# Kernel optimization log

Measured on AMD Instinct MI355X. Metric: run time of the kernel, lower is better.

Reference implementation:

```python
import jax, jax.numpy as jnp
import numpy as np

EPS = 1e-5

def conv3x3(x, w, b=None):
    # NCHW, OIHW, stride 1, padding 1
    y = jax.lax.conv_general_dilated(x, w, (1, 1), ((1, 1), (1, 1)),
                                     dimension_numbers=('NCHW', 'OIHW', 'NCHW'))
    if b is not None:
        y = y + b[None, :, None, None]
    return y

def batchnorm(x, g, b):
    # training-mode BN (PyTorch default): biased variance over (N,H,W)
    m = x.mean((0, 2, 3), keepdims=True)
    v = x.var((0, 2, 3), keepdims=True)
    return (x - m) * jax.lax.rsqrt(v + EPS) * g[None, :, None, None] + b[None, :, None, None]

def upsample2x_align_corners(x):
    # bilinear, align_corners=True, scale_factor=2
    def lerp_axis(a, Lin, axis):
        Lout = 2 * Lin
        c = jnp.arange(Lout, dtype=a.dtype) * (Lin - 1) / (Lout - 1)
        i0 = jnp.floor(c).astype(jnp.int32)
        i1 = jnp.minimum(i0 + 1, Lin - 1)
        w = c - i0.astype(a.dtype)
        shape = [1] * a.ndim
        shape[axis] = Lout
        w = w.reshape(shape)
        return jnp.take(a, i0, axis=axis) * (1 - w) + jnp.take(a, i1, axis=axis) * w
    x = lerp_axis(x, x.shape[2], 2)
    x = lerp_axis(x, x.shape[3], 3)
    return x

def deform_sample(x, offsets):
    # torchvision DeformConv2d v1 sampling: kernel 3x3, pad 1, offsets [B,18,H,W]
    # layout: per kernel point k (row-major), channels (2k, 2k+1) = (dy, dx)
    B, C, H, W = x.shape
    K = 9
    off = offsets.reshape(B, K, 2, H, W)
    ky, kx = jnp.meshgrid(jnp.arange(3) - 1, jnp.arange(3) - 1, indexing='ij')
    ky = ky.reshape(K).astype(x.dtype)
    kx = kx.reshape(K).astype(x.dtype)
    gy = jnp.arange(H, dtype=x.dtype)[None, None, :, None]
    gx = jnp.arange(W, dtype=x.dtype)[None, None, None, :]
    py = gy + ky[None, :, None, None] + off[:, :, 0]  # [B,K,H,W]
    px = gx + kx[None, :, None, None] + off[:, :, 1]
    y0 = jnp.floor(py)
    x0 = jnp.floor(px)
    wy = (py - y0)[:, None]  # [B,1,K,H,W]
    wx = (px - x0)[:, None]
    y0i = y0.astype(jnp.int32)
    x0i = x0.astype(jnp.int32)
    x_flat = x.reshape(B, C, H * W)
    def gather(yi, xi):
        valid = ((yi >= 0) & (yi < H) & (xi >= 0) & (xi < W))
        idx = jnp.clip(yi, 0, H - 1) * W + jnp.clip(xi, 0, W - 1)  # [B,K,H,W]
        g = jnp.take_along_axis(x_flat, idx.reshape(B, 1, K * H * W), axis=2)
        return g.reshape(B, C, K, H, W) * valid[:, None].astype(x.dtype)
    v00 = gather(y0i, x0i)
    v01 = gather(y0i, x0i + 1)
    v10 = gather(y0i + 1, x0i)
    v11 = gather(y0i + 1, x0i + 1)
    return (v00 * (1 - wy) * (1 - wx) + v01 * (1 - wy) * wx
            + v10 * wy * (1 - wx) + v11 * wy * wx)

def setup_inputs() -> dict:
    key = jax.random.key(0)
    ks = jax.random.split(key, 6)
    B, in_ch, skip_ch, out_ch = 4, 256, 128, 128
    Hs, Ws = 128, 128
    x = jax.random.normal(ks[0], (B, in_ch, Hs // 2, Ws // 2), jnp.float32)
    skip = jax.random.normal(ks[1], (B, skip_ch, Hs, Ws), jnp.float32)
    cat_ch = in_ch + skip_ch
    conv1_w = jax.random.normal(ks[2], (out_ch, cat_ch, 3, 3), jnp.float32) * (2.0 / (cat_ch * 9)) ** 0.5
    off_w = jax.random.normal(ks[3], (18, out_ch, 3, 3), jnp.float32) * 0.01
    off_b = jnp.zeros((18,), jnp.float32)
    def_w = jax.random.normal(ks[4], (out_ch, out_ch, 3, 3), jnp.float32) * (2.0 / (out_ch * 9)) ** 0.5
    def_b = jnp.zeros((out_ch,), jnp.float32)
    return {
        'x': x, 'skip': skip,
        'conv1_w': conv1_w,
        'bn1_g': jnp.ones((out_ch,), jnp.float32), 'bn1_b': jnp.zeros((out_ch,), jnp.float32),
        'off_w': off_w, 'off_b': off_b,
        'def_w': def_w, 'def_b': def_b,
        'bn2_g': jnp.ones((out_ch,), jnp.float32), 'bn2_b': jnp.zeros((out_ch,), jnp.float32),
    }

def reference(x, skip, conv1_w, bn1_g, bn1_b, off_w, off_b, def_w, def_b, bn2_g, bn2_b):
    xu = upsample2x_align_corners(x)
    dh = skip.shape[2] - xu.shape[2]
    dw = skip.shape[3] - xu.shape[3]
    if dh != 0 or dw != 0:
        xu = jnp.pad(xu, ((0, 0), (0, 0), (dh // 2, dh - dh // 2), (dw // 2, dw - dw // 2)))
    cat = jnp.concatenate([skip, xu], axis=1)
    h = jax.nn.relu(batchnorm(conv3x3(cat, conv1_w), bn1_g, bn1_b))
    offsets = conv3x3(h, off_w, off_b)  # [B,18,H,W]
    sampled = deform_sample(h, offsets)  # [B,C,9,H,W]
    O = def_w.shape[0]
    y = jnp.einsum('ock,bckhw->bohw', def_w.reshape(O, def_w.shape[1], 9), sampled)
    y = y + def_b[None, :, None, None]
    return jax.nn.relu(batchnorm(y, bn2_g, bn2_b))
```

## Files before the change

### kernel.cpp

```cpp
#include <hip/hip_runtime.h>
#include <hip/hip_bf16.h>

typedef __hip_bfloat16 bf16;
typedef __bf16 bf16x8 __attribute__((ext_vector_type(8)));
typedef __bf16 bf16x4 __attribute__((ext_vector_type(4)));
typedef float  f32x4  __attribute__((ext_vector_type(4)));

constexpr int NB   = 4;
constexpr int H    = 128;
constexpr int W    = 128;
constexpr int HW   = H * W;
constexpr int NPIX = NB * HW;
constexpr int CCAT = 384;
constexpr int CSKIP= 128;
constexpr int CIN  = 256;
constexpr int CO   = 128;
constexpr int HS   = 64;
constexpr int WP   = 130;
constexpr int K1   = 3456;
constexpr int KD   = 1152;
constexpr int NBORD= 2 * WP + 2 * (WP - 2);
constexpr float EPS = 1e-5f;

__device__ __forceinline__ float b2f(bf16 v){ return __bfloat162float(v); }
__device__ __forceinline__ bf16  f2b(float v){ return __float2bfloat16(v); }

__device__ __forceinline__ void async_copy16(const void* g, void* s){
    __builtin_amdgcn_global_load_lds((const __attribute__((address_space(1))) void*)g,
                                     (__attribute__((address_space(3))) void*)s, 16, 0, 0);
}

__device__ __forceinline__ void border_yx(int p, int& y, int& x){
    if (p < WP)             { y = 0;        x = p; }
    else if (p < 2 * WP)    { y = WP - 1;   x = p - WP; }
    else if (p < 2 * WP + (WP - 2)) { y = p - 2 * WP + 1;          x = 0; }
    else                    { y = p - (2 * WP + (WP - 2)) + 1;     x = WP - 1; }
}

__global__ void k_prep(float* __restrict__ sums, bf16* __restrict__ catp,
                       bf16* __restrict__ hp){
    int i = blockIdx.x * blockDim.x + threadIdx.x;
    int stride = gridDim.x * blockDim.x;
    for (int j = i; j < 512; j += stride) sums[j] = 0.f;
    const int nCat = NB * NBORD * CCAT;
    for (int j = i; j < nCat; j += stride){
        int c = j % CCAT, r = j / CCAT, p = r % NBORD, b = r / NBORD;
        int y, x; border_yx(p, y, x);
        catp[(((size_t)b * WP + y) * WP + x) * CCAT + c] = f2b(0.f);
    }
    const int nHp = NB * NBORD * CO;
    for (int j = i; j < nHp; j += stride){
        int c = j % CO, r = j / CO, p = r % NBORD, b = r / NBORD;
        int y, x; border_yx(p, y, x);
        hp[(((size_t)b * WP + y) * WP + x) * CO + c] = f2b(0.f);
    }
}

__global__ __launch_bounds__(256) void k_build_cat2(const float* __restrict__ x,
                                                    const float* __restrict__ skip,
                                                    bf16* __restrict__ catp){
    constexpr int TS = 66;
    __shared__ bf16 tile[128 * TS];
    int t  = threadIdx.x;
    int y  = blockIdx.x % H, b = blockIdx.x / H;
    int xx = t & 127, cp = t >> 7;

    float cy = (y * 63.0f) / 127.0f;
    int   y0 = (int)cy;
    int   y1 = min(y0 + 1, HS - 1);
    float wy = cy - y0;
    float cxf = (xx * 63.0f) / 127.0f;
    int   x0 = (int)cxf;
    int   x1 = min(x0 + 1, HS - 1);
    float wx = cxf - x0;

    bf16* orow = catp + (((size_t)b * WP + y + 1) * WP + 1) * CCAT;

    for (int chunk = 0; chunk < 6; chunk++){
        int cbase = chunk * 64;
        if (chunk >= 1) __syncthreads();
        if (chunk < 2){
            const float* sb = skip + ((size_t)(b * CSKIP + cbase + cp * 32) * H + y) * W;
#pragma unroll
            for (int i = 0; i < 32; i++)
                tile[xx * TS + cp * 32 + i] = f2b(sb[(size_t)i * HW + xx]);
        } else {
            int icb = (chunk - 2) * 64 + cp * 32;
            const float* xr0 = x + ((size_t)(b * CIN + icb) * HS + y0) * HS;
            const float* xr1 = x + ((size_t)(b * CIN + icb) * HS + y1) * HS;
#pragma unroll
            for (int i = 0; i < 32; i++){
                const float* r0 = xr0 + (size_t)i * HS * HS;
                const float* r1 = xr1 + (size_t)i * HS * HS;
                float v0 = r0[x0] * (1 - wx) + r0[x1] * wx;
                float v1 = r1[x0] * (1 - wx) + r1[x1] * wx;
                tile[xx * TS + cp * 32 + i] = f2b(v0 * (1 - wy) + v1 * wy);
            }
        }
        __syncthreads();
        int cc2 = (t & 31) * 2;
        int px0 = t >> 5;
#pragma unroll
        for (int pp = 0; pp < 16; pp++){
            int px = pp * 8 + px0;
            unsigned int v = *(const unsigned int*)&tile[px * TS + cc2];
            *(unsigned int*)&orow[(size_t)px * CCAT + cbase + cc2] = v;
        }
    }
}

__global__ void k_tr_all(const float* __restrict__ w1, const float* __restrict__ wo,
                         const float* __restrict__ wd,
                         bf16* __restrict__ wt1, bf16* __restrict__ wto,
                         bf16* __restrict__ wtd){
    int i = blockIdx.x * blockDim.x + threadIdx.x;
    if (i < CO * K1){
        int k = i % K1, oc = i / K1;
        int ky = k / 1152, r = k % 1152, kx = r / 384, ic = r % 384;
        wt1[i] = f2b(w1[((oc * CCAT + ic) * 3 + ky) * 3 + kx]);
        return;
    }
    i -= CO * K1;
    if (i < 32 * KD){
        int kk = i % KD, o = i / KD;
        int ky = kk / 384, r = kk % 384, kx = r >> 7, ic = r & 127;
        wto[i] = (o < 18) ? f2b(wo[((o * CO + ic) * 3 + ky) * 3 + kx]) : f2b(0.f);
        return;
    }
    i -= 32 * KD;
    if (i < CO * KD){
        int kk = i % KD, o = i / KD;
        int kp = kk >> 7, c = kk & 127;
        wtd[i] = f2b(wd[(o * CO + c) * 9 + kp]);
    }
}

__global__ __launch_bounds__(512) void k_conv1_mfma(const bf16* __restrict__ catp,
                                                    const bf16* __restrict__ wbt,
                                                    bf16* __restrict__ hp,
                                                    float* __restrict__ sums){
    __shared__ unsigned short Ab[256 * 64];
    __shared__ unsigned short Bb[128 * 64];
    __shared__ float ps[256];
    int t = threadIdx.x;
    int l = t & 63, w = t >> 6;
    int y0 = (blockIdx.x & 63) * 2, b = blockIdx.x >> 6;

    int pr   = l >> 3;
    int koct = (l & 7) ^ pr;
    int m    = l & 15, quad = l >> 4;
    int wm   = w & 3,  wn   = w >> 2;

    f32x4 acc[4][4];
#pragma unroll
    for (int i = 0; i < 4; i++)
#pragma unroll
        for (int j = 0; j < 4; j++) acc[i][j] = f32x4{0.f, 0.f, 0.f, 0.f};

    const size_t rowStride = (size_t)WP * CCAT;
    const bf16* Abase = catp + ((size_t)(b * WP) + y0) * rowStride;

    for (int ky = 0; ky < 3; ky++){
        for (int kc = 0; kc < 18; kc++){
            int c0 = kc / 6, r0 = (kc % 6) * 64;
            __syncthreads();
#pragma unroll
            for (int i = 0; i < 4; i++){
                int pxg = i * 64 + w * 8;
                int rr  = pxg >> 7;
                int xl  = (pxg & 127) + pr;
                const bf16* Arow = Abase + (size_t)(rr + ky) * rowStride;
                async_copy16(Arow + (size_t)(xl + c0) * CCAT + r0 + koct * 8,
                             &Ab[pxg * 64]);
            }
            int kg = ky * 1152 + kc * 64;
#pragma unroll
            for (int i = 0; i < 2; i++){
                int ocg = i * 64 + w * 8;
                async_copy16(wbt + (size_t)(ocg + pr) * K1 + kg + koct * 8,
                             &Bb[ocg * 64]);
            }
            __syncthreads();
            const bf16x8* ap = (const bf16x8*)Ab;
            const bf16x8* bp = (const bf16x8*)Bb;
#pragma unroll
            for (int ks = 0; ks < 2; ks++){
                bf16x8 af[4], bfr[4];
#pragma unroll
                for (int mi = 0; mi < 4; mi++){
                    int px = wm * 64 + mi * 16 + m;
                    af[mi] = ap[px * 8 + ((ks * 4 + quad) ^ (px & 7))];
                }
#pragma unroll
                for (int ni = 0; ni < 4; ni++){
                    int oc = wn * 64 + ni * 16 + m;
                    bfr[ni] = bp[oc * 8 + ((ks * 4 + quad) ^ (oc & 7))];
                }
#pragma unroll
                for (int mi = 0; mi < 4; mi++)
#pragma unroll
                    for (int ni = 0; ni < 4; ni++)
                        acc[mi][ni] = __builtin_amdgcn_mfma_f32_16x16x32_bf16(
                            af[mi], bfr[ni], acc[mi][ni], 0, 0, 0);
            }
        }
    }
#pragma unroll
    for (int mi = 0; mi < 4; mi++){
        int p0 = wm * 64 + mi * 16 + quad * 4;
        size_t obase = (((size_t)b * WP + y0 + (p0 >> 7) + 1) * WP + 1 + (p0 & 127)) * CO;
#pragma unroll
        for (int ni = 0; ni < 4; ni++){
            int oc = wn * 64 + ni * 16 + m;
#pragma unroll
            for (int r = 0; r < 4; r++)
                hp[obase + (size_t)r * CO + oc] = f2b(acc[mi][ni][r]);
        }
    }
    if (t < 256) ps[t] = 0.f;
    __syncthreads();
#pragma unroll
    for (int ni = 0; ni < 4; ni++){
        int ch = wn * 64 + ni * 16 + m;
        float s = 0.f, q = 0.f;
#pragma unroll
        for (int mi = 0; mi < 4; mi++)
#pragma unroll
            for (int r = 0; r < 4; r++){
                float v = acc[mi][ni][r];
                s += v; q += v * v;
            }
        s += __shfl_xor(s, 16); s += __shfl_xor(s, 32);
        q += __shfl_xor(q, 16); q += __shfl_xor(q, 32);
        if (quad == 0){
            atomicAdd(&ps[ch], s);
            atomicAdd(&ps[128 + ch], q);
        }
    }
    __syncthreads();
    if (t < 128){
        atomicAdd(&sums[t],       ps[t]);
        atomicAdd(&sums[128 + t], ps[128 + t]);
    }
}

__global__ __launch_bounds__(256) void k_bn_apply_pad(bf16* __restrict__ t,
                                                      const float* __restrict__ sums,
                                                      const float* __restrict__ g,
                                                      const float* __restrict__ bb){
    __shared__ float ssc[256];
    int tt = threadIdx.x;
    if (tt < 128){
        float mean = sums[tt] / (float)NPIX;
        float var  = sums[128 + tt] / (float)NPIX - mean * mean;
        float scale = g[tt] * rsqrtf(var + EPS);
        ssc[tt]       = scale;
        ssc[128 + tt] = bb[tt] - mean * scale;
    }
    __syncthreads();
    int i = blockIdx.x * 256 + tt;
    if (i >= NPIX * CO) return;
    int c = i & 127;
    int pix = i >> 7;
    int xw = pix & 127, yh = (pix >> 7) & 127, b = pix >> 14;
    size_t a = (((size_t)b * WP + yh + 1) * WP + xw + 1) * CO + c;
    float v = b2f(t[a]) * ssc[c] + ssc[128 + c];
    t[a] = f2b(v > 0.f ? v : 0.f);
}

__global__ __launch_bounds__(256) void k_conv_off_mfma(const bf16* __restrict__ hp,
                                                       const bf16* __restrict__ wob,
                                                       const float* __restrict__ off_b,
                                                       bf16* __restrict__ offs){
    __shared__ unsigned short Ab[128 * 64];
    __shared__ unsigned short Bb[32 * 64];
    int t = threadIdx.x, l = t & 63, w = t >> 6;
    int y = blockIdx.x % H, b = blockIdx.x / H;
    int pr = l >> 3, koct = (l & 7) ^ pr;
    int m = l & 15, quad = l >> 4;
    int wm = w & 1, wn = w >> 1;

    f32x4 acc[4];
#pragma unroll
    for (int i = 0; i < 4; i++) acc[i] = f32x4{0.f, 0.f, 0.f, 0.f};

    const size_t rowStride = (size_t)WP * CO;
    for (int ky = 0; ky < 3; ky++){
        const bf16* Arow = hp + ((size_t)(b * WP) + y + ky) * rowStride;
        for (int kc = 0; kc < 6; kc++){
            int kx = kc >> 1, r0 = (kc & 1) * 64;
            __syncthreads();
#pragma unroll
            for (int i = 0; i < 4; i++){
                int px = w * 32 + i * 8 + pr;
                async_copy16(Arow + (size_t)(px + kx) * CO + r0 + koct * 8,
                             &Ab[(w * 32 + i * 8) * 64]);
            }
            int kg = ky * 384 + kx * 128 + r0;
            async_copy16(wob + (size_t)(w * 8 + pr) * KD + kg + koct * 8,
                         &Bb[(w * 8) * 64]);
            __syncthreads();
            const bf16x8* ap = (const bf16x8*)Ab;
            const bf16x8* bp = (const bf16x8*)Bb;
#pragma unroll
            for (int ks = 0; ks < 2; ks++){
                int oc = wn * 16 + m;
                bf16x8 bfr = bp[oc * 8 + ((ks * 4 + quad) ^ (oc & 7))];
#pragma unroll
                for (int mi = 0; mi < 4; mi++){
                    int px = wm * 64 + mi * 16 + m;
                    bf16x8 af = ap[px * 8 + ((ks * 4 + quad) ^ (px & 7))];
                    acc[mi] = __builtin_amdgcn_mfma_f32_16x16x32_bf16(af, bfr, acc[mi], 0, 0, 0);
                }
            }
        }
    }
    int oc = wn * 16 + m;
    if (oc < 18){
        float bias = off_b[oc];
        int rowpix = b * HW + y * W;
#pragma unroll
        for (int mi = 0; mi < 4; mi++){
            int p0 = wm * 64 + mi * 16 + quad * 4;
#pragma unroll
            for (int r = 0; r < 4; r++)
                offs[(size_t)(rowpix + p0 + r) * 18 + oc] = f2b(acc[mi][r] + bias);
        }
    }
}

__global__ __launch_bounds__(256) void k_deform_mfma(const bf16* __restrict__ hp,
                                                     const bf16* __restrict__ offs,
                                                     const bf16* __restrict__ wdb,
                                                     const float* __restrict__ def_b,
                                                     bf16* __restrict__ y,
                                                     float* __restrict__ sums){
    __shared__ unsigned short Ab[128 * 64];
    __shared__ unsigned short Bb[128 * 64];
    __shared__ int2   sc_yx[9 * 128];
    __shared__ float4 sc_w[9 * 128];
    __shared__ float  ps[256];

    int t = threadIdx.x, l = t & 63, w = t >> 6;
    int yrow = blockIdx.x % H, b = blockIdx.x / H;
    int rowpix = b * HW + yrow * W;

    for (int idx = t; idx < 9 * 128; idx += 256){
        int kp = idx >> 7, px = idx & 127;
        float dy = b2f(offs[(size_t)(rowpix + px) * 18 + 2 * kp]);
        float dx = b2f(offs[(size_t)(rowpix + px) * 18 + 2 * kp + 1]);
        float py = yrow + (kp / 3 - 1) + dy;
        float pxx = px + (kp % 3 - 1) + dx;
        float fy = floorf(py), fx = floorf(pxx);
        float wy = py - fy, wx = pxx - fx;
        int y0 = (int)fy, x0 = (int)fx;
        bool vy0 = (y0 >= 0) && (y0 < H);
        bool vy1 = (y0 + 1 >= 0) && (y0 + 1 < H);
        bool vx0 = (x0 >= 0) && (x0 < W);
        bool vx1 = (x0 + 1 >= 0) && (x0 + 1 < W);
        int y0c = min(max(y0, 0), H - 1),     y1c = min(max(y0 + 1, 0), H - 1);
        int x0c = min(max(x0, 0), W - 1),     x1c = min(max(x0 + 1, 0), W - 1);
        sc_yx[idx] = make_int2(((y0c + 1) * WP) | (((y1c + 1) * WP) << 16),
                               (x0c + 1) | ((x1c + 1) << 16));
        sc_w[idx] = make_float4((1 - wy) * (1 - wx) * (float)(vy0 && vx0),
                                (1 - wy) * wx       * (float)(vy0 && vx1),
                                wy * (1 - wx)       * (float)(vy1 && vx0),
                                wy * wx             * (float)(vy1 && vx1));
    }
    __syncthreads();

    int pr = l >> 3, koct = (l & 7) ^ pr;
    int m = l & 15, quad = l >> 4;
    int wm = w & 1, wn = w >> 1;
    int g = l >> 4, j = l & 15;

    f32x4 acc[4][4];
#pragma unroll
    for (int i = 0; i < 4; i++)
#pragma unroll
        for (int jj = 0; jj < 4; jj++) acc[i][jj] = f32x4{0.f, 0.f, 0.f, 0.f};

    const bf16* hpb = hp + (size_t)b * WP * WP * CO;

    for (int kc = 0; kc < 18; kc++){
        int kp = kc >> 1, ch = (kc & 1) * 64;
        __syncthreads();
        int kg = kp * 128 + ch;
#pragma unroll
        for (int i = 0; i < 4; i++){
            int oc = w * 32 + i * 8 + pr;
            async_copy16(wdb + (size_t)oc * KD + kg + koct * 8,
                         &Bb[(w * 32 + i * 8) * 64]);
        }
        int cb = ch + j * 4;
#pragma unroll
        for (int p = 0; p < 8; p++){
            int px = w * 32 + g * 8 + p;
            int idx = kp * 128 + px;
            int2 yx = sc_yx[idx];
            float4 w4 = sc_w[idx];
            int r0 = yx.x & 0xffff, r1 = ((unsigned)yx.x) >> 16;
            int c0 = yx.y & 0xffff, c1 = ((unsigned)yx.y) >> 16;
            const bf16* base = hpb + cb;
            bf16x4 s00 = *(const bf16x4*)(base + (size_t)(r0 + c0) * CO);
            bf16x4 s01 = *(const bf16x4*)(base + (size_t)(r0 + c1) * CO);
            bf16x4 s10 = *(const bf16x4*)(base + (size_t)(r1 + c0) * CO);
            bf16x4 s11 = *(const bf16x4*)(base + (size_t)(r1 + c1) * CO);
            bf16x4 pv;
#pragma unroll
            for (int r = 0; r < 4; r++){
                float v = w4.x * (float)s00[r] + w4.y * (float)s01[r]
                        + w4.z * (float)s10[r] + w4.w * (float)s11[r];
                pv[r] = (__bf16)v;
            }
            int oct_sw = (j >> 1) ^ (px & 7);
            *(bf16x4*)&Ab[px * 64 + oct_sw * 8 + (j & 1) * 4] = pv;
        }
        __syncthreads();
        const bf16x8* ap = (const bf16x8*)Ab;
        const bf16x8* bp = (const bf16x8*)Bb;
#pragma unroll
        for (int ks = 0; ks < 2; ks++){
            bf16x8 af[4], bfr[4];
#pragma unroll
            for (int mi = 0; mi < 4; mi++){
                int px = wm * 64 + mi * 16 + m;
                af[mi] = ap[px * 8 + ((ks * 4 + quad) ^ (px & 7))];
            }
#pragma unroll
            for (int ni = 0; ni < 4; ni++){
                int oc = wn * 64 + ni * 16 + m;
                bfr[ni] = bp[oc * 8 + ((ks * 4 + quad) ^ (oc & 7))];
            }
#pragma unroll
            for (int mi = 0; mi < 4; mi++)
#pragma unroll
                for (int ni = 0; ni < 4; ni++)
                    acc[mi][ni] = __builtin_amdgcn_mfma_f32_16x16x32_bf16(
                        af[mi], bfr[ni], acc[mi][ni], 0, 0, 0);
        }
    }
#pragma unroll
    for (int mi = 0; mi < 4; mi++){
        int p0 = wm * 64 + mi * 16 + quad * 4;
#pragma unroll
        for (int ni = 0; ni < 4; ni++){
            int oc = wn * 64 + ni * 16 + m;
            float bias = def_b[oc];
#pragma unroll
            for (int r = 0; r < 4; r++)
                y[(size_t)(rowpix + p0 + r) * CO + oc] = f2b(acc[mi][ni][r] + bias);
        }
    }
    ps[t] = 0.f;
    __syncthreads();
#pragma unroll
    for (int ni = 0; ni < 4; ni++){
        int ch = wn * 64 + ni * 16 + m;
        float bias = def_b[ch];
        float s = 0.f, q = 0.f;
#pragma unroll
        for (int mi = 0; mi < 4; mi++)
#pragma unroll
            for (int r = 0; r < 4; r++){
                float v = acc[mi][ni][r] + bias;
                s += v; q += v * v;
            }
        s += __shfl_xor(s, 16); s += __shfl_xor(s, 32);
        q += __shfl_xor(q, 16); q += __shfl_xor(q, 32);
        if (quad == 0){
            atomicAdd(&ps[ch], s);
            atomicAdd(&ps[128 + ch], q);
        }
    }
    __syncthreads();
    if (t < 128){
        atomicAdd(&sums[t],       ps[t]);
        atomicAdd(&sums[128 + t], ps[128 + t]);
    }
}

__global__ __launch_bounds__(256) void k_final(const bf16* __restrict__ yb,
                                               const float* __restrict__ sums,
                                               const float* __restrict__ g,
                                               const float* __restrict__ bb,
                                               float* __restrict__ out){
    __shared__ unsigned short tile[128 * 129];
    __shared__ float ssc[256];
    int t = threadIdx.x;
    if (t < 128){
        float mean = sums[t] / (float)NPIX;
        float var  = sums[128 + t] / (float)NPIX - mean * mean;
        float scale = g[t] * rsqrtf(var + EPS);
        ssc[t]       = scale;
        ssc[128 + t] = bb[t] - mean * scale;
    }
    int yrow = blockIdx.x % H, b = blockIdx.x / H;
    int rowbase = b * HW + yrow * W;
    const unsigned short* src = (const unsigned short*)yb;
    for (int it = 0; it < 64; it++){
        int idx = it * 256 + t;
        int c = idx & 127, px = idx >> 7;
        tile[px * 129 + c] = src[(size_t)(rowbase + px) * CO + c];
    }
    __syncthreads();
    for (int it = 0; it < 64; it++){
        int idx = it * 256 + t;
        int xw = idx & 127, o = idx >> 7;
        unsigned short u = tile[xw * 129 + o];
        float v = (float)(*(const __bf16*)&u);
        v = v * ssc[o] + ssc[128 + o];
        out[(((size_t)b * CO + o) * H + yrow) * W + xw] = v > 0.f ? v : 0.f;
    }
}

extern "C" void kernel_launch(void* const* d_in, const int* in_sizes, int n_in,
                              void* d_out, int out_size, void* d_ws, size_t ws_size,
                              hipStream_t stream){
    const float* x      = (const float*)d_in[0];
    const float* skip   = (const float*)d_in[1];
    const float* conv1w = (const float*)d_in[2];
    const float* bn1g   = (const float*)d_in[3];
    const float* bn1b   = (const float*)d_in[4];
    const float* offw   = (const float*)d_in[5];
    const float* offb   = (const float*)d_in[6];
    const float* defw   = (const float*)d_in[7];
    const float* defb   = (const float*)d_in[8];
    const float* bn2g   = (const float*)d_in[9];
    const float* bn2b   = (const float*)d_in[10];
    float* out = (float*)d_out;

    char* ws = (char*)d_ws;
    size_t off_bytes = 0;
    auto alloc = [&](size_t bytes) -> void* {
        void* p = ws + off_bytes;
        off_bytes += (bytes + 255) & ~(size_t)255;
        return p;
    };
    const size_t catp_elems = (size_t)NB * WP * WP * CCAT;
    const size_t hp_elems   = (size_t)NB * WP * WP * CO;
    bf16*  catp  = (bf16*) alloc(catp_elems * 2);
    bf16*  hp    = (bf16*) alloc(hp_elems * 2);
    bf16*  offs  = (bf16*) alloc((size_t)NPIX * 18 * 2);
    bf16*  yb    = (bf16*) alloc((size_t)NPIX * CO * 2);
    bf16*  wbt   = (bf16*) alloc((size_t)CO * K1 * 2);
    bf16*  wob   = (bf16*) alloc((size_t)32 * KD * 2);
    bf16*  wdb   = (bf16*) alloc((size_t)CO * KD * 2);
    float* sums  = (float*)alloc(512 * 4);
    float* sums1 = sums;
    float* sums2 = sums + 256;

    k_prep<<<1024, 256, 0, stream>>>(sums, catp, hp);

    k_build_cat2<<<NB * H, 256, 0, stream>>>(x, skip, catp);

    const int ntr = CO * K1 + 32 * KD + CO * KD;
    k_tr_all<<<(ntr + 255) / 256, 256, 0, stream>>>(conv1w, offw, defw, wbt, wob, wdb);

    k_conv1_mfma<<<NB * H / 2, 512, 0, stream>>>(catp, wbt, hp, sums1);

    k_bn_apply_pad<<<(NPIX * CO + 255) / 256, 256, 0, stream>>>(hp, sums1, bn1g, bn1b);

    k_conv_off_mfma<<<NB * H, 256, 0, stream>>>(hp, wob, offb, offs);

    k_deform_mfma<<<NB * H, 256, 0, stream>>>(hp, offs, wdb, defb, yb, sums2);

    k_final<<<NB * H, 256, 0, stream>>>(yb, sums2, bn2g, bn2b, out);
}
```

Baseline: 359.3 us.

## Reuse haloed input row across kx taps in conv1 and offset conv

Both implicit-GEMM convolutions now load one padded input row (130 pixels plus a channel chunk) into shared memory once per ky/channel-chunk, then slide the pixel index by kx to cover all three horizontal taps. Previously each tap reloaded a separate A tile. This cuts global/LDS load traffic for activations about threefold. conv1 also changes from 512-thread blocks over two rows to 256-thread blocks over one row, and the offset conv loads all three kx weight slices at once. The cost is less parallelism per block, more barriers for the conv1 weight tiles, and larger LDS use.

```diff
diff --git a/kernel.cpp b/kernel.cpp
--- a/kernel.cpp
+++ b/kernel.cpp
@@ -135,21 +135,21 @@
     }
 }
 
-__global__ __launch_bounds__(512) void k_conv1_mfma(const bf16* __restrict__ catp,
+__global__ __launch_bounds__(256) void k_conv1_mfma(const bf16* __restrict__ catp,
                                                     const bf16* __restrict__ wbt,
                                                     bf16* __restrict__ hp,
                                                     float* __restrict__ sums){
-    __shared__ unsigned short Ab[256 * 64];
+    __shared__ unsigned short Ab[132 * 128];
     __shared__ unsigned short Bb[128 * 64];
     __shared__ float ps[256];
     int t = threadIdx.x;
     int l = t & 63, w = t >> 6;
-    int y0 = (blockIdx.x & 63) * 2, b = blockIdx.x >> 6;
+    int y = blockIdx.x % H, b = blockIdx.x / H;
 
     int pr   = l >> 3;
     int koct = (l & 7) ^ pr;
     int m    = l & 15, quad = l >> 4;
-    int wm   = w & 3,  wn   = w >> 2;
+    int wm   = w & 1,  wn   = w >> 1;
 
     f32x4 acc[4][4];
 #pragma unroll
@@ -158,66 +158,68 @@
         for (int j = 0; j < 4; j++) acc[i][j] = f32x4{0.f, 0.f, 0.f, 0.f};
 
     const size_t rowStride = (size_t)WP * CCAT;
-    const bf16* Abase = catp + ((size_t)(b * WP) + y0) * rowStride;
-
     for (int ky = 0; ky < 3; ky++){
-        for (int kc = 0; kc < 18; kc++){
-            int c0 = kc / 6, r0 = (kc % 6) * 64;
+        const bf16* Arow = catp + ((size_t)(b * WP) + y + ky) * rowStride;
+        for (int ci = 0; ci < 3; ci++){
             __syncthreads();
-#pragma unroll
-            for (int i = 0; i < 4; i++){
-                int pxg = i * 64 + w * 8;
-                int rr  = pxg >> 7;
-                int xl  = (pxg & 127) + pr;
-                const bf16* Arow = Abase + (size_t)(rr + ky) * rowStride;
-                async_copy16(Arow + (size_t)(xl + c0) * CCAT + r0 + koct * 8,
-                             &Ab[pxg * 64]);
-            }
-            int kg = ky * 1152 + kc * 64;
-#pragma unroll
-            for (int i = 0; i < 2; i++){
-                int ocg = i * 64 + w * 8;
-                async_copy16(wbt + (size_t)(ocg + pr) * K1 + kg + koct * 8,
-                             &Bb[ocg * 64]);
-            }
-            __syncthreads();
-            const bf16x8* ap = (const bf16x8*)Ab;
-            const bf16x8* bp = (const bf16x8*)Bb;
-#pragma unroll
-            for (int ks = 0; ks < 2; ks++){
-                bf16x8 af[4], bfr[4];
-#pragma unroll
-                for (int mi = 0; mi < 4; mi++){
-                    int px = wm * 64 + mi * 16 + m;
-                    af[mi] = ap[px * 8 + ((ks * 4 + quad) ^ (px & 7))];
+            for (int i = w; i < 33; i += 4){
+                int G  = i * 64 + l;
+                int px = G >> 4, ol = G & 15;
+                int osrc = ol ^ (px & 7);
+                async_copy16(Arow + (size_t)px * CCAT + ci * 128 + osrc * 8,
+                             &Ab[i * 512]);
+            }
+            for (int kx = 0; kx < 3; kx++){
+                for (int s64 = 0; s64 < 2; s64++){
+                    if (kx | s64) __syncthreads();
+                    int kg = ky * 1152 + kx * 384 + ci * 128 + s64 * 64;
+#pragma unroll
+                    for (int i = 0; i < 4; i++){
+                        int ocg = w * 32 + i * 8;
+                        async_copy16(wbt + (size_t)(ocg + pr) * K1 + kg + koct * 8,
+                                     &Bb[ocg * 64]);
+                    }
+                    __syncthreads();
+                    const bf16x8* ap = (const bf16x8*)Ab;
+                    const bf16x8* bp = (const bf16x8*)Bb;
+#pragma unroll
+                    for (int ks = 0; ks < 2; ks++){
+                        int s = s64 * 2 + ks;
+                        bf16x8 af[4], bfr[4];
+#pragma unroll
+                        for (int mi = 0; mi < 4; mi++){
+                            int pxk = wm * 64 + mi * 16 + m + kx;
+                            af[mi] = ap[pxk * 16 + ((s * 4 + quad) ^ (pxk & 7))];
+                        }
+#pragma unroll
+                        for (int ni = 0; ni < 4; ni++){
+                            int oc = wn * 64 + ni * 16 + m;
+                            bfr[ni] = bp[oc * 8 + ((ks * 4 + quad) ^ (oc & 7))];
+                        }
+#pragma unroll
+                        for (int mi = 0; mi < 4; mi++)
+#pragma unroll
+                            for (int ni = 0; ni < 4; ni++)
+                                acc[mi][ni] = __builtin_amdgcn_mfma_f32_16x16x32_bf16(
+                                    af[mi], bfr[ni], acc[mi][ni], 0, 0, 0);
+                    }
                 }
-#pragma unroll
-                for (int ni = 0; ni < 4; ni++){
-                    int oc = wn * 64 + ni * 16 + m;
-                    bfr[ni] = bp[oc * 8 + ((ks * 4 + quad) ^ (oc & 7))];
-                }
-#pragma unroll
-                for (int mi = 0; mi < 4; mi++)
-#pragma unroll
-                    for (int ni = 0; ni < 4; ni++)
-                        acc[mi][ni] = __builtin_amdgcn_mfma_f32_16x16x32_bf16(
-                            af[mi], bfr[ni], acc[mi][ni], 0, 0, 0);
-            }
-        }
-    }
+            }
+        }
+    }
+    size_t obase = (((size_t)b * WP + y + 1) * WP + 1) * CO;
 #pragma unroll
     for (int mi = 0; mi < 4; mi++){
         int p0 = wm * 64 + mi * 16 + quad * 4;
-        size_t obase = (((size_t)b * WP + y0 + (p0 >> 7) + 1) * WP + 1 + (p0 & 127)) * CO;
 #pragma unroll
         for (int ni = 0; ni < 4; ni++){
             int oc = wn * 64 + ni * 16 + m;
 #pragma unroll
             for (int r = 0; r < 4; r++)
-                hp[obase + (size_t)r * CO + oc] = f2b(acc[mi][ni][r]);
-        }
-    }
-    if (t < 256) ps[t] = 0.f;
+                hp[obase + (size_t)(p0 + r) * CO + oc] = f2b(acc[mi][ni][r]);
+        }
+    }
+    ps[t] = 0.f;
     __syncthreads();
 #pragma unroll
     for (int ni = 0; ni < 4; ni++){
@@ -272,11 +274,10 @@
                                                        const bf16* __restrict__ wob,
                                                        const float* __restrict__ off_b,
                                                        bf16* __restrict__ offs){
-    __shared__ unsigned short Ab[128 * 64];
-    __shared__ unsigned short Bb[32 * 64];
+    __shared__ unsigned short Ab[132 * 128];
+    __shared__ unsigned short Bb[32 * 384];
     int t = threadIdx.x, l = t & 63, w = t >> 6;
     int y = blockIdx.x % H, b = blockIdx.x / H;
-    int pr = l >> 3, koct = (l & 7) ^ pr;
     int m = l & 15, quad = l >> 4;
     int wm = w & 1, wn = w >> 1;
 
@@ -284,32 +285,35 @@
 #pragma unroll
     for (int i = 0; i < 4; i++) acc[i] = f32x4{0.f, 0.f, 0.f, 0.f};
 
-    const size_t rowStride = (size_t)WP * CO;
+    const size_t rowStrideH = (size_t)WP * CO;
     for (int ky = 0; ky < 3; ky++){
-        const bf16* Arow = hp + ((size_t)(b * WP) + y + ky) * rowStride;
-        for (int kc = 0; kc < 6; kc++){
-            int kx = kc >> 1, r0 = (kc & 1) * 64;
-            __syncthreads();
-#pragma unroll
-            for (int i = 0; i < 4; i++){
-                int px = w * 32 + i * 8 + pr;
-                async_copy16(Arow + (size_t)(px + kx) * CO + r0 + koct * 8,
-                             &Ab[(w * 32 + i * 8) * 64]);
-            }
-            int kg = ky * 384 + kx * 128 + r0;
-            async_copy16(wob + (size_t)(w * 8 + pr) * KD + kg + koct * 8,
-                         &Bb[(w * 8) * 64]);
-            __syncthreads();
-            const bf16x8* ap = (const bf16x8*)Ab;
-            const bf16x8* bp = (const bf16x8*)Bb;
-#pragma unroll
-            for (int ks = 0; ks < 2; ks++){
+        const bf16* Arow = hp + ((size_t)(b * WP) + y + ky) * rowStrideH;
+        __syncthreads();
+        for (int i = w; i < 33; i += 4){
+            int G  = i * 64 + l;
+            int px = G >> 4, ol = G & 15;
+            int osrc = ol ^ (px & 7);
+            async_copy16(Arow + (size_t)px * CO + osrc * 8, &Ab[i * 512]);
+        }
+        for (int i = w; i < 24; i += 4){
+            int g  = i * 64 + l;
+            int kx = g >> 9, oc = (g >> 4) & 31, ol = g & 15;
+            int osrc = ol ^ (oc & 7);
+            async_copy16(wob + (size_t)oc * KD + ky * 384 + kx * 128 + osrc * 8,
+                         &Bb[i * 512]);
+        }
+        __syncthreads();
+        const bf16x8* ap = (const bf16x8*)Ab;
+        const bf16x8* bp = (const bf16x8*)Bb;
+        for (int kx = 0; kx < 3; kx++){
+#pragma unroll
+            for (int s = 0; s < 4; s++){
                 int oc = wn * 16 + m;
-                bf16x8 bfr = bp[oc * 8 + ((ks * 4 + quad) ^ (oc & 7))];
+                bf16x8 bfr = bp[kx * 512 + oc * 16 + ((s * 4 + quad) ^ (oc & 7))];
 #pragma unroll
                 for (int mi = 0; mi < 4; mi++){
-                    int px = wm * 64 + mi * 16 + m;
-                    bf16x8 af = ap[px * 8 + ((ks * 4 + quad) ^ (px & 7))];
+                    int pxk = wm * 64 + mi * 16 + m + kx;
+                    bf16x8 af = ap[pxk * 16 + ((s * 4 + quad) ^ (pxk & 7))];
                     acc[mi] = __builtin_amdgcn_mfma_f32_16x16x32_bf16(af, bfr, acc[mi], 0, 0, 0);
                 }
             }
@@ -557,7 +561,7 @@
     const int ntr = CO * K1 + 32 * KD + CO * KD;
     k_tr_all<<<(ntr + 255) / 256, 256, 0, stream>>>(conv1w, offw, defw, wbt, wob, wdb);
 
-    k_conv1_mfma<<<NB * H / 2, 512, 0, stream>>>(catp, wbt, hp, sums1);
+    k_conv1_mfma<<<NB * H, 256, 0, stream>>>(catp, wbt, hp, sums1);
 
     k_bn_apply_pad<<<(NPIX * CO + 255) / 256, 256, 0, stream>>>(hp, sums1, bn1g, bn1b);
 
```

Measured after the change: 334.6 us. 6.9% less time.
